# Kernel optimization log

Hardware: AMD Instinct MI355X
Metric: run time of the kernel (lower is better)

The kernel has to match this reference:

```python
import jax, jax.numpy as jnp
import numpy as np

SHIFT = 1  # shift_direction fixed to +1 (original picks +/-1 randomly at init)

def setup_inputs() -> dict:
    key = jax.random.key(0)
    k1, k2, k3 = jax.random.split(key, 3)
    x  = jax.random.normal(k1, (1024, 1792, 28), dtype=jnp.float32)
    w0 = jax.random.normal(k2, (128, 2), dtype=jnp.float32)
    w1 = jax.random.normal(k3, (64, 3, 128), dtype=jnp.float32)
    return {"x": x, "w0": w0, "w1": w1}

def reference(x, w0, w1):
    # unfold (im2col) with kernel (3,1), padding (1,0) along the 28-dim
    xp = jnp.pad(x, ((0, 0), (0, 0), (1, 1)))                 # (1024,1792,30)
    patches = jnp.stack([xp[:, :, k:k + 28] for k in range(3)], axis=2)  # (1024,1792,3,28)
    t3 = patches.reshape(1024, 64, 28, 3, 28)                 # (l,j,m,k,n)
    # einsum 'ljmnk,jki->lmni' (t3 here is in (l,j,m,k,n) order)
    t4 = jnp.einsum('ljmkn,jki->lmni', t3, w1)                # (1024,28,28,128)
    # outer product with w0, directly in the permuted (k,l,i,m,j) order
    t5 = jnp.einsum('klmi,ij->klimj', t4, w0)                 # (1024,28,128,28,2)
    t6 = t5.reshape(1024, 28, 128, 56)
    t6 = jnp.roll(t6, SHIFT, axis=3)
    t6 = t6.reshape(1024, 28, 128, 28, 2).sum(axis=4)         # (1024,28,128,28)
    t7 = jnp.roll(t6, SHIFT, axis=1)
    y = jnp.transpose(t7, (0, 2, 3, 1))                       # (1024,128,28,28)
    return y
```

## Files before the change

### kernel.cpp

```cpp
#include <hip/hip_runtime.h>

typedef short bf16x8 __attribute__((ext_vector_type(8)));
typedef float f32x4 __attribute__((ext_vector_type(4)));
typedef unsigned short u16x4 __attribute__((ext_vector_type(4)));

__device__ __forceinline__ unsigned short f2b(float f) {
    unsigned int u = __builtin_bit_cast(unsigned int, f);
    u += 0x7fffu + ((u >> 16) & 1u);
    return (unsigned short)(u >> 16);
}
__device__ __forceinline__ float b2f(unsigned short s) {
    unsigned int u = ((unsigned int)s) << 16;
    return __builtin_bit_cast(float, u);
}

__global__ void wt_prepass(const float* __restrict__ w1, unsigned short* __restrict__ wt) {
    int t = blockIdx.x * 256 + threadIdx.x;
    if (t >= 24576) return;
    int j = t & 63;
    int i = (t >> 6) & 127;
    int k = t >> 13;
    wt[t] = f2b(w1[(j * 3 + k) * 128 + i]);
}


__global__ __launch_bounds__(512, 4) void fused_main(
        const float* __restrict__ x, const float* __restrict__ w0,
        const unsigned short* __restrict__ wt, float* __restrict__ y) {
    __shared__ __align__(16) char smem[65536];
    __shared__ float w0s[256];

    const int tid  = threadIdx.x;
    const int lane = tid & 63;
    const int w    = tid >> 6;
    const int rl   = lane & 15;
    const int jb0  = (lane >> 4) << 3;

    const int B   = (int)blockIdx.x;
    const int b   = ((B & 7) << 7) + ((B >> 3) >> 2);
    const int bc  = (B >> 3) & 3;
    const int c0  = 7 * bc;

    if (tid < 256) w0s[tid] = w0[tid];

    {
        int nh = (bc == 0) ? 2 : ((bc == 3) ? 1 : 0);
        for (int idx = tid; idx < nh * 224; idx += 512) {
            int rr = idx;
            int sl;
            if (bc == 0) {
                if (rr >= 224) { sl = 11; rr -= 224; } else sl = 0;
            } else {
                sl = 9;
            }
            int a   = rr >> 3, ch = rr & 7;
            int row = a * 13 + sl;
            int byte = (row << 7) + ((ch << 4) ^ ((row & 7) << 4));
            *reinterpret_cast<f32x4*>(smem + byte) = f32x4{0.f, 0.f, 0.f, 0.f};
        }
    }

    int q0, q1, q2;
    if      (bc == 0) { q0 = 0; q1 = 1; q2 = 6; }
    else if (bc == 1) { q0 = 1; q1 = 2; q2 = 3; }
    else if (bc == 2) { q0 = 3; q1 = 4; q2 = 5; }
    else              { q0 = 4; q1 = 5; q2 = 6; }

    const float* xb = x + (size_t)b * (1792 * 28);
#pragma unroll
    for (int sb = 0; sb < 2; ++sb) {
        const int u0 = sb * 3;
        float4 v0[3], v1[3];
#pragma unroll
        for (int u = 0; u < 3; ++u) {
            int P = tid + ((u0 + u) << 9);
            if (P < 2688) {
                int rp = P / 3, q3 = P - rp * 3;
                int q  = (q3 == 0) ? q0 : ((q3 == 1) ? q1 : q2);
                int a  = rp % 28, jp = rp / 28;
                const float* p0 = xb + (jp * 56 + a) * 28 + (q << 2);
                v0[u] = *reinterpret_cast<const float4*>(p0);
                v1[u] = *reinterpret_cast<const float4*>(p0 + 784);
            }
        }
#pragma unroll
        for (int u = 0; u < 3; ++u) {
            int P = tid + ((u0 + u) << 9);
            if (P < 2688) {
                int rp = P / 3, q3 = P - rp * 3;
                int q  = (q3 == 0) ? q0 : ((q3 == 1) ? q1 : q2);
                int a  = rp % 28, jp = rp / 28;
                int a13 = a * 13;
                int j4  = jp << 2;
                float lo4[4] = {v0[u].x, v0[u].y, v0[u].z, v0[u].w};
                float hi4[4] = {v1[u].x, v1[u].y, v1[u].z, v1[u].w};
#pragma unroll
                for (int e = 0; e < 4; ++e) {
                    int n = (q << 2) + e;
                    int sl; bool ok;
                    if (bc == 0) {
                        if (n < 8)        { sl = n + 1;  ok = true; }
                        else if (n >= 26) { sl = n - 17; ok = true; }
                        else              { sl = 0;      ok = false; }
                    } else {
                        sl = n + 2 - c0;
                        ok = (unsigned)sl < 10u;
                    }
                    if (ok) {
                        int row  = a13 + sl;
                        int byte = (row << 7) + (j4 ^ ((row & 7) << 4));
                        unsigned int pk;
                        asm("v_cvt_pk_bf16_f32 %0, %1, %2" : "=v"(pk) : "v"(lo4[e]), "v"(hi4[e]));
                        *(unsigned int*)(smem + byte) = pk;
                    }
                }
            }
        }
    }
    __syncthreads();

    const int cl  = rl & 7;
    const int rh  = rl >> 3;
    const int mt0 = (w >> 2) * 7;
    const int wn  = w & 3;
    int rowoff[3];
#pragma unroll
    for (int k = 0; k < 3; ++k) {
        int sIdx = (bc == 0) ? ((cl == 0) ? (9 + k) : (cl - 1 + k)) : (cl + k);
        rowoff[k] = rh * 13 + sIdx;
    }

    f32x4 acc[7][2];
#pragma unroll
    for (int mt = 0; mt < 7; ++mt) {
        acc[mt][0] = f32x4{0.f, 0.f, 0.f, 0.f};
        acc[mt][1] = f32x4{0.f, 0.f, 0.f, 0.f};
    }

#pragma unroll
    for (int s = 0; s < 6; ++s) {
        const int k  = s >> 1;
        const int jb = ((s & 1) << 5) + jb0;
        const int jx = jb << 1;
        bf16x8 b0 = *reinterpret_cast<const bf16x8*>(wt + (k << 13) + (((wn << 5) + rl) << 6) + jb);
        bf16x8 b1 = *reinterpret_cast<const bf16x8*>(wt + (k << 13) + (((wn << 5) + 16 + rl) << 6) + jb);
#pragma unroll
        for (int mt = 0; mt < 7; ++mt) {
            int row  = 26 * (mt0 + mt) + rowoff[k];
            int byte = (row << 7) + (jx ^ ((row & 7) << 4));
            bf16x8 af = *reinterpret_cast<const bf16x8*>(smem + byte);
            acc[mt][0] = __builtin_amdgcn_mfma_f32_16x16x32_bf16(af, b0, acc[mt][0], 0, 0, 0);
            acc[mt][1] = __builtin_amdgcn_mfma_f32_16x16x32_bf16(af, b1, acc[mt][1], 0, 0, 0);
        }
    }
    __syncthreads();

    {
        const int rq  = (lane >> 4) << 2;
        const int icb = (wn << 5) + rl;
#pragma unroll
        for (int mt = 0; mt < 7; ++mt) {
            int rbase = ((mt0 + mt) << 4) + rq;
            int a     = rbase >> 3;
            int l     = (a == 27) ? 0 : (a + 1);
            int l2    = l << 1;
            int clb   = rbase & 7;
#pragma unroll
            for (int p = 0; p < 2; ++p) {
                int ic   = icb + (p << 4);
                int base = (ic << 9);
                int ic7  = ic * 7;
#pragma unroll
                for (int q = 0; q < 4; ++q) {
                    int cc   = clb + q;
                    int byte = base + (cc << 6) + (l2 ^ (((ic7 + cc) & 7) << 3));
                    *(unsigned short*)(smem + byte) = f2b(acc[mt][p][q]);
                }
            }
        }
    }
    __syncthreads();

#pragma unroll
    for (int u = 0; u < 13; ++u) {
        int f = tid + (u << 9);
        if (f < 6272) {
            int lq    = f % 7;
            int t1    = f / 7;
            int m_loc = t1 % 7;
            int iloc  = t1 / 7;
            float w00 = w0s[2 * iloc], w01 = w0s[2 * iloc + 1];
            int m     = c0 + m_loc;
            int lo    = lq << 3;
            int i7    = iloc * 7;
            int cl1   = m_loc + 1;
            int cl2   = m_loc;
            int by1   = (iloc << 9) + (cl1 << 6) + (lo ^ (((i7 + cl1) & 7) << 3));
            int by2   = (iloc << 9) + (cl2 << 6) + (lo ^ (((i7 + cl2) & 7) << 3));
            u16x4 h1  = *reinterpret_cast<const u16x4*>(smem + by1);
            u16x4 h2  = *reinterpret_cast<const u16x4*>(smem + by2);
            f32x4 o;
            o.x = w00 * b2f(h1.x) + w01 * b2f(h2.x);
            o.y = w00 * b2f(h1.y) + w01 * b2f(h2.y);
            o.z = w00 * b2f(h1.z) + w01 * b2f(h2.z);
            o.w = w00 * b2f(h1.w) + w01 * b2f(h2.w);
            __builtin_nontemporal_store(
                o, reinterpret_cast<f32x4*>(y + ((((size_t)b * 128 + iloc) * 28 + m) * 28) + (lq << 2)));
        }
    }
}

extern "C" void kernel_launch(void* const* d_in, const int* in_sizes, int n_in,
                              void* d_out, int out_size, void* d_ws, size_t ws_size,
                              hipStream_t stream) {
    const float* x  = (const float*)d_in[0];
    const float* w0 = (const float*)d_in[1];
    const float* w1 = (const float*)d_in[2];
    float* y = (float*)d_out;
    unsigned short* wt = (unsigned short*)d_ws;

    hipLaunchKernelGGL(wt_prepass, dim3(96), dim3(256), 0, stream, w1, wt);
    hipLaunchKernelGGL(fused_main, dim3(4096), dim3(512), 0, stream, x, w0, wt, y);
}
```

Measured before the change: 153.5 us.

## Restructure epilogue LDS layout to packed column-major rows with vectorized reads

Changes the epilogue staging layout in shared memory so that each output channel's eight consecutive columns for a given l are packed together (464-byte stride per channel). Accumulators are written as packed 64-bit pairs instead of 16-bit scalar stores, and each thread in the final pass reads four 16-byte vectors once, then produces all seven m outputs from registers. This is meant to cut LDS store and load instruction counts and the redundant double reads of neighbouring columns. The unswizzled 464-byte stride may bring bank conflicts, and fewer threads now do more work each (896 work items instead of 6272).

```diff
diff --git a/kernel.cpp b/kernel.cpp
--- a/kernel.cpp
+++ b/kernel.cpp
@@ -2,16 +2,19 @@
 
 typedef short bf16x8 __attribute__((ext_vector_type(8)));
 typedef float f32x4 __attribute__((ext_vector_type(4)));
-typedef unsigned short u16x4 __attribute__((ext_vector_type(4)));
+typedef unsigned int u32x2 __attribute__((ext_vector_type(2)));
+typedef unsigned int u32x4 __attribute__((ext_vector_type(4)));
 
 __device__ __forceinline__ unsigned short f2b(float f) {
     unsigned int u = __builtin_bit_cast(unsigned int, f);
     u += 0x7fffu + ((u >> 16) & 1u);
     return (unsigned short)(u >> 16);
 }
-__device__ __forceinline__ float b2f(unsigned short s) {
-    unsigned int u = ((unsigned int)s) << 16;
-    return __builtin_bit_cast(float, u);
+__device__ __forceinline__ float hi2f(unsigned int u) {
+    return __builtin_bit_cast(float, u & 0xffff0000u);
+}
+__device__ __forceinline__ float lo2f(unsigned int u) {
+    return __builtin_bit_cast(float, u << 16);
 }
 
 __global__ void wt_prepass(const float* __restrict__ w1, unsigned short* __restrict__ wt) {
@@ -163,49 +166,54 @@
             int rbase = ((mt0 + mt) << 4) + rq;
             int a     = rbase >> 3;
             int l     = (a == 27) ? 0 : (a + 1);
-            int l2    = l << 1;
             int clb   = rbase & 7;
+            int lofs  = (l << 4) + (clb << 1);
 #pragma unroll
             for (int p = 0; p < 2; ++p) {
-                int ic   = icb + (p << 4);
-                int base = (ic << 9);
-                int ic7  = ic * 7;
-#pragma unroll
-                for (int q = 0; q < 4; ++q) {
-                    int cc   = clb + q;
-                    int byte = base + (cc << 6) + (l2 ^ (((ic7 + cc) & 7) << 3));
-                    *(unsigned short*)(smem + byte) = f2b(acc[mt][p][q]);
+                int ic = icb + (p << 4);
+                unsigned int pk0 = (unsigned int)f2b(acc[mt][p][0])
+                                 | ((unsigned int)f2b(acc[mt][p][1]) << 16);
+                unsigned int pk1 = (unsigned int)f2b(acc[mt][p][2])
+                                 | ((unsigned int)f2b(acc[mt][p][3]) << 16);
+                u32x2 pk; pk.x = pk0; pk.y = pk1;
+                *reinterpret_cast<u32x2*>(smem + ic * 464 + lofs) = pk;
+            }
+        }
+    }
+    __syncthreads();
+
+#pragma unroll
+    for (int u = 0; u < 2; ++u) {
+        int f = tid + (u << 9);
+        if (f < 896) {
+            int lq   = f % 7;
+            int iloc = f / 7;
+            float w00 = w0s[2 * iloc], w01 = w0s[2 * iloc + 1];
+            const char* base = smem + iloc * 464 + (lq << 6);
+            u32x4 v_[4];
+#pragma unroll
+            for (int u4 = 0; u4 < 4; ++u4)
+                v_[u4] = *reinterpret_cast<const u32x4*>(base + (u4 << 4));
+            float* yb = y + (size_t)b * 100352 + (size_t)iloc * 784 + c0 * 28 + (lq << 2);
+#pragma unroll
+            for (int m = 0; m < 7; ++m) {
+                f32x4 o;
+#pragma unroll
+                for (int u4 = 0; u4 < 4; ++u4) {
+                    float cm, cm1;
+                    if ((m & 1) == 0) {
+                        unsigned int wd = v_[u4][m >> 1];
+                        cm  = lo2f(wd);
+                        cm1 = hi2f(wd);
+                    } else {
+                        cm  = hi2f(v_[u4][m >> 1]);
+                        cm1 = lo2f(v_[u4][(m + 1) >> 1]);
+                    }
+                    o[u4] = w00 * cm1 + w01 * cm;
                 }
-            }
-        }
-    }
-    __syncthreads();
-
-#pragma unroll
-    for (int u = 0; u < 13; ++u) {
-        int f = tid + (u << 9);
-        if (f < 6272) {
-            int lq    = f % 7;
-            int t1    = f / 7;
-            int m_loc = t1 % 7;
-            int iloc  = t1 / 7;
-            float w00 = w0s[2 * iloc], w01 = w0s[2 * iloc + 1];
-            int m     = c0 + m_loc;
-            int lo    = lq << 3;
-            int i7    = iloc * 7;
-            int cl1   = m_loc + 1;
-            int cl2   = m_loc;
-            int by1   = (iloc << 9) + (cl1 << 6) + (lo ^ (((i7 + cl1) & 7) << 3));
-            int by2   = (iloc << 9) + (cl2 << 6) + (lo ^ (((i7 + cl2) & 7) << 3));
-            u16x4 h1  = *reinterpret_cast<const u16x4*>(smem + by1);
-            u16x4 h2  = *reinterpret_cast<const u16x4*>(smem + by2);
-            f32x4 o;
-            o.x = w00 * b2f(h1.x) + w01 * b2f(h2.x);
-            o.y = w00 * b2f(h1.y) + w01 * b2f(h2.y);
-            o.z = w00 * b2f(h1.z) + w01 * b2f(h2.z);
-            o.w = w00 * b2f(h1.w) + w01 * b2f(h2.w);
-            __builtin_nontemporal_store(
-                o, reinterpret_cast<f32x4*>(y + ((((size_t)b * 128 + iloc) * 28 + m) * 28) + (lq << 2)));
+                __builtin_nontemporal_store(
+                    o, reinterpret_cast<f32x4*>(yb + m * 28));
+            }
         }
     }
 }
```

After: 219.3 us. +42.9%, slower.
